# Kernel optimization log

Measured on AMD Instinct MI355X. Metric: run time of the kernel, lower is better.

The kernel has to match this reference:

```python
import jax, jax.numpy as jnp
import numpy as np

N_USER, N_ITEM, D, N_LAYER, NNZ, B = 50000, 100000, 64, 3, 2400000, 4096
NEG_SLOPE = 0.2
EPS = 1e-12


def setup_inputs() -> dict:
    key = jax.random.key(0)
    ks = jax.random.split(key, 12)
    N = N_USER + N_ITEM
    user_emb = jax.random.normal(ks[0], (N_USER, D), dtype=jnp.float32) * 0.1
    item_emb = jax.random.normal(ks[1], (N_ITEM, D), dtype=jnp.float32) * 0.1
    rows = jax.random.randint(ks[2], (NNZ,), 0, N, dtype=jnp.int32)
    cols = jax.random.randint(ks[3], (NNZ,), 0, N, dtype=jnp.int32)
    edge_index = jnp.stack([rows, cols])  # [2, nnz] COO indices of sparse L
    # normalized-Laplacian-like positive values, ~1/deg scale
    edge_vals = jax.random.uniform(ks[4], (NNZ,), dtype=jnp.float32) * (1.0 / 16.0)
    scale = 1.0 / np.sqrt(D)
    W1 = jax.random.normal(ks[5], (N_LAYER, D, D), dtype=jnp.float32) * scale
    W2 = jax.random.normal(ks[6], (N_LAYER, D, D), dtype=jnp.float32) * scale
    b1 = jnp.zeros((N_LAYER, D), dtype=jnp.float32)
    b2 = jnp.zeros((N_LAYER, D), dtype=jnp.float32)
    users = jax.random.randint(ks[7], (B,), 1, N_USER + 1, dtype=jnp.int32)      # 1-indexed
    pos_items = jax.random.randint(ks[8], (B,), 1, N_ITEM + 1, dtype=jnp.int32)  # 1-indexed
    neg_items = jax.random.randint(ks[9], (B,), 1, N_ITEM + 1, dtype=jnp.int32)  # 1-indexed
    return {"user_emb": user_emb, "item_emb": item_emb, "edge_vals": edge_vals,
            "W1": W1, "b1": b1, "W2": W2, "b2": b2,
            "edge_index": edge_index, "users": users,
            "pos_items": pos_items, "neg_items": neg_items}


def _spmm(rows, cols, vals, E, num_nodes):
    # sparse COO L @ E : gather source rows, scale by edge value, scatter-add to dest rows
    return jax.ops.segment_sum(vals[:, None] * E[cols], rows, num_segments=num_nodes)


def reference(user_emb, item_emb, edge_vals, W1, b1, W2, b2,
              edge_index, users, pos_items, neg_items):
    n_user = user_emb.shape[0]
    N = n_user + item_emb.shape[0]
    rows, cols = edge_index[0], edge_index[1]
    E = jnp.concatenate([user_emb, item_emb], axis=0)  # [N, d]
    all_E = [E]
    for i in range(W1.shape[0]):
        LE = _spmm(rows, cols, edge_vals, E, N)          # L @ E
        # (L + I) @ E @ W1 + (L@E * E) @ W2  (dropouts are eval-mode identity)
        h = (LE + E) @ W1[i] + b1[i] + (LE * E) @ W2[i] + b2[i]
        E = jax.nn.leaky_relu(h, NEG_SLOPE)
        nrm = jnp.maximum(jnp.linalg.norm(E, axis=1, keepdims=True), EPS)
        all_E.append(E / nrm)  # L2-normalized copy stored; unnormalized E propagates
    all_E = jnp.concatenate(all_E, axis=1)               # [N, d*(1+L)]
    u_emb = all_E[:n_user][users - 1]
    items = all_E[n_user:]
    return u_emb, items[pos_items - 1], items[neg_items - 1]
```

## Files before the change

### kernel.cpp

```cpp
#include <hip/hip_runtime.h>

#define N_USERC 50000
#define N_ITEMC 100000
#define NN      150000
#define DD      64
#define NLAYER  3
#define NNZC    2400000
#define BB      4096
#define NRID    (3*BB)
#define NBKT    147
#define NABLK   586
#define NTILE   4688
#define ELLW    32
#define ELLROWS 150528
#define OVCAP   32768
#define NZBLK   9408

typedef unsigned short ushort_t;
typedef __attribute__((ext_vector_type(8))) short bf16x8;
typedef __attribute__((ext_vector_type(4))) float f32x4;

static __device__ __forceinline__ float bf2f(ushort_t b) {
    unsigned int u = ((unsigned int)b) << 16;
    return __uint_as_float(u);
}
static __device__ __forceinline__ ushort_t f2bf(float f) {
    unsigned int u = __float_as_uint(f);
    u = u + 0x7FFFu + ((u >> 16) & 1u);
    return (ushort_t)(u >> 16);
}

__global__ __launch_bounds__(256) void k_sniffzb(const unsigned int* __restrict__ ue_words,
                                                 int* __restrict__ flag,
                                                 int* __restrict__ bucket_cnt) {
    int t = threadIdx.x;
    if (t < 64) {
        int cnt = 0;
        for (int i = 0; i < 4; i++) {
            unsigned int w = ue_words[t * 4 + i];
            unsigned int lo = w & 0xFFFFu;
            unsigned int ex = (lo >> 7) & 0xFF;
            if (ex >= 100 && ex <= 132) cnt++;
        }
        for (int m = 1; m < 64; m <<= 1) cnt += __shfl_xor(cnt, m, 64);
        if (t == 0) *flag = (cnt >= 128) ? 1 : 0;
    } else if (t - 64 < NBKT) {
        bucket_cnt[t - 64] = 0;
    }
}

__global__ __launch_bounds__(256) void k_zell(int4* __restrict__ ell4,
                                              int* __restrict__ ovcnt) {
    int idx = blockIdx.x * 256 + threadIdx.x;
    ell4[idx] = make_int4(0, 0, 0, 0);
    if (idx == 0) *ovcnt = 0;
}

__global__ __launch_bounds__(256) void k_init2(const void* __restrict__ ue,
                                               const void* __restrict__ ie,
                                               const int* __restrict__ flag,
                                               float* __restrict__ E,
                                               ushort_t* __restrict__ Eb0) {
    int idx = blockIdx.x * 256 + threadIdx.x;
    if (idx >= NN * DD) return;
    int row = idx >> 6;
    bool isU = row < N_USERC;
    int si = isU ? idx : idx - N_USERC * DD;
    float v;
    if (*flag) {
        v = bf2f(isU ? ((const ushort_t*)ue)[si] : ((const ushort_t*)ie)[si]);
    } else {
        v = isU ? ((const float*)ue)[si] : ((const float*)ie)[si];
    }
    E[idx] = v;
    Eb0[idx] = f2bf(v);
}

__global__ __launch_bounds__(256) void k_wprep(const void* __restrict__ W1,
                                               const void* __restrict__ W2,
                                               const void* __restrict__ b1,
                                               const void* __restrict__ b2,
                                               const int* __restrict__ flag,
                                               ushort_t* __restrict__ Wfrag,
                                               float* __restrict__ bsum) {
    int idx = blockIdx.x * 256 + threadIdx.x;
    int isbf = *flag;
    if (idx < NLAYER * 4 * 4 * 64 * 8) {
        int i    = idx & 7;
        int lane = (idx >> 3) & 63;
        int jt   = (idx >> 9) & 3;
        int s    = (idx >> 11) & 3;
        int l    = idx >> 13;
        int kfull = 32 * (s & 1) + 8 * (lane >> 4) + i;
        int col   = jt * 16 + (lane & 15);
        const void* W = (s < 2) ? W1 : W2;
        size_t off = (size_t)l * 4096 + (size_t)kfull * 64 + col;
        float v = isbf ? bf2f(((const ushort_t*)W)[off]) : ((const float*)W)[off];
        Wfrag[idx] = f2bf(v);
    } else {
        int r = idx - NLAYER * 4 * 4 * 64 * 8;
        if (r < NLAYER * 64) {
            float v1 = isbf ? bf2f(((const ushort_t*)b1)[r]) : ((const float*)b1)[r];
            float v2 = isbf ? bf2f(((const ushort_t*)b2)[r]) : ((const float*)b2)[r];
            bsum[r] = v1 + v2;
        }
    }
}

__global__ __launch_bounds__(256) void k_bhist(const int* __restrict__ rows,
                                               int* __restrict__ bucket_cnt) {
    __shared__ int h[NBKT];
    int t = threadIdx.x;
    if (t < NBKT) h[t] = 0;
    __syncthreads();
    int e0 = blockIdx.x * 4096;
#pragma unroll
    for (int i = 0; i < 16; i++) {
        int e = e0 + t + i * 256;
        if (e < NNZC) atomicAdd(&h[rows[e] >> 10], 1);
    }
    __syncthreads();
    if (t < NBKT && h[t]) atomicAdd(&bucket_cnt[t], h[t]);
}

__global__ __launch_bounds__(256) void k_bscan(const int* __restrict__ bucket_cnt,
                                               int* __restrict__ gbase,
                                               int* __restrict__ gcursor) {
    __shared__ int s[256];
    int t = threadIdx.x;
    int v = (t < NBKT) ? bucket_cnt[t] : 0;
    s[t] = v; __syncthreads();
    for (int off = 1; off < 256; off <<= 1) {
        int x = (t >= off) ? s[t - off] : 0;
        __syncthreads();
        s[t] += x;
        __syncthreads();
    }
    if (t < NBKT) { int ex = s[t] - v; gbase[t] = ex; gcursor[t] = ex; }
    if (t == 0) { gbase[NBKT] = NNZC; }
}

__global__ __launch_bounds__(256) void k_phaseA(const int* __restrict__ rows,
                                                const int* __restrict__ cols,
                                                const void* __restrict__ vals,
                                                const int* __restrict__ flag,
                                                int* __restrict__ gcursor,
                                                int2* __restrict__ binned) {
    __shared__ int hist[NBKT], base_[NBKT], lcur[NBKT];
    int t = threadIdx.x;
    int e0 = blockIdx.x * 4096;
    if (t < NBKT) { hist[t] = 0; lcur[t] = 0; }
    __syncthreads();
    int myrow[16];
#pragma unroll
    for (int i = 0; i < 16; i++) {
        int e = e0 + t + i * 256;
        int r = -1;
        if (e < NNZC) { r = rows[e]; atomicAdd(&hist[r >> 10], 1); }
        myrow[i] = r;
    }
    __syncthreads();
    if (t < NBKT && hist[t] > 0) base_[t] = atomicAdd(&gcursor[t], hist[t]);
    __syncthreads();
    int isbf = *flag;
#pragma unroll
    for (int i = 0; i < 16; i++) {
        int e = e0 + t + i * 256;
        if (e < NNZC) {
            int r = myrow[i];
            int bkt = r >> 10;
            int off = atomicAdd(&lcur[bkt], 1);
            int pos = base_[bkt] + off;
            int c = cols[e];
            float v = isbf ? bf2f(((const ushort_t*)vals)[e]) : ((const float*)vals)[e];
            binned[pos] = make_int2(((r & 1023) << 18) | c, __float_as_int(v));
        }
    }
}

__global__ __launch_bounds__(256) void k_phaseB(const int* __restrict__ gbase,
                                                const int2* __restrict__ binned,
                                                int2* __restrict__ ell,
                                                int4* __restrict__ ovbuf,
                                                int* __restrict__ ovcnt) {
    __shared__ int rcur[1024];
    int b = blockIdx.x, t = threadIdx.x;
    int s = gbase[b], e = gbase[b + 1];
    for (int i = t; i < 1024; i += 256) rcur[i] = 0;
    __syncthreads();
    for (int i = s + t; i < e; i += 256) {
        int2 en = binned[i];
        int rl = en.x >> 18;
        int c  = en.x & 0x3FFFF;
        int off = atomicAdd(&rcur[rl], 1);
        if (off < ELLW) {
            ell[((size_t)(b * 1024 + rl)) * ELLW + off] = make_int2(c, en.y);
        } else {
            int p = atomicAdd(ovcnt, 1);
            if (p < OVCAP) ovbuf[p] = make_int4(b * 1024 + rl, c, en.y, 0);
        }
    }
}

__global__ __launch_bounds__(256) void k_layer(const int2* __restrict__ ell,
                                               const int4* __restrict__ ovbuf,
                                               const int* __restrict__ ovcnt,
                                               const ushort_t* __restrict__ Eb_in,
                                               float* __restrict__ E,
                                               ushort_t* __restrict__ Eb_out,
                                               const ushort_t* __restrict__ Wfrag,
                                               const float* __restrict__ bsum,
                                               int layer) {
    __shared__ float sLE[32][68];
    __shared__ float sE [32][68];

    int t    = threadIdx.x;
    int wv   = t >> 6;
    int lane = t & 63;
    int oct  = lane >> 3;
    int d8   = (lane & 7) * 8;
    int hl   = lane >> 4;
    int l16  = lane & 15;
    int r0   = blockIdx.x << 5;

    {
        int lr = t >> 3;
        int dm = (t & 7) * 8;
        int gr = r0 + lr;
        float4 va = make_float4(0.f, 0.f, 0.f, 0.f), vb = va;
        if (gr < NN) {
            const float4* p = (const float4*)(E + (size_t)gr * DD + dm);
            va = p[0]; vb = p[1];
        }
        *(float4*)&sE[lr][dm]     = va;
        *(float4*)&sE[lr][dm + 4] = vb;
    }

    int baseRow = r0 + wv * 8;
    int2 pv[4];
#pragma unroll
    for (int v = 0; v < 4; v++)
        pv[v] = ell[(size_t)baseRow * ELLW + v * 8 + oct];

#pragma unroll
    for (int sub = 0; sub < 8; sub++) {
        uint4 q[4];
#pragma unroll
        for (int v = 0; v < 4; v++)
            q[v] = *(const uint4*)(Eb_in + ((size_t)(unsigned)pv[v].x << 6) + d8);
        int2 pvn[4];
        if (sub < 7) {
#pragma unroll
            for (int v = 0; v < 4; v++)
                pvn[v] = ell[(size_t)(baseRow + sub + 1) * ELLW + v * 8 + oct];
        }
        float acc[8];
#pragma unroll
        for (int k = 0; k < 8; k++) acc[k] = 0.f;
#pragma unroll
        for (int v = 0; v < 4; v++) {
            float w = __int_as_float(pv[v].y);
            acc[0] = fmaf(w, __uint_as_float(q[v].x << 16),         acc[0]);
            acc[1] = fmaf(w, __uint_as_float(q[v].x & 0xffff0000u), acc[1]);
            acc[2] = fmaf(w, __uint_as_float(q[v].y << 16),         acc[2]);
            acc[3] = fmaf(w, __uint_as_float(q[v].y & 0xffff0000u), acc[3]);
            acc[4] = fmaf(w, __uint_as_float(q[v].z << 16),         acc[4]);
            acc[5] = fmaf(w, __uint_as_float(q[v].z & 0xffff0000u), acc[5]);
            acc[6] = fmaf(w, __uint_as_float(q[v].w << 16),         acc[6]);
            acc[7] = fmaf(w, __uint_as_float(q[v].w & 0xffff0000u), acc[7]);
        }
#pragma unroll
        for (int m = 8; m < 64; m <<= 1)
#pragma unroll
            for (int k = 0; k < 8; k++) acc[k] += __shfl_xor(acc[k], m, 64);
        if (oct == 0) {
            int lr = wv * 8 + sub;
            *(float4*)&sLE[lr][d8]     = make_float4(acc[0], acc[1], acc[2], acc[3]);
            *(float4*)&sLE[lr][d8 + 4] = make_float4(acc[4], acc[5], acc[6], acc[7]);
        }
#pragma unroll
        for (int v = 0; v < 4; v++) pv[v] = pvn[v];
    }
    __syncthreads();

    {
        int n = *ovcnt;
        n = (n < OVCAP) ? n : OVCAP;
        if (wv == 0) {
            for (int i = 0; i < n; i++) {
                int4 ov = ovbuf[i];
                if ((unsigned)(ov.x - r0) < 32u) {
                    float w = __int_as_float(ov.z);
                    sLE[ov.x - r0][lane] += w * bf2f(Eb_in[(size_t)ov.y * DD + lane]);
                }
            }
        }
    }
    __syncthreads();

    int rt = wv & 1;
    int j0w = wv >> 1;
    int jtA = 2 * j0w, jtB = 2 * j0w + 1;
    const uint4* wb = (const uint4*)(Wfrag + (size_t)layer * 8192);
    float bsA = bsum[layer * 64 + jtA * 16 + l16];
    float bsB = bsum[layer * 64 + jtB * 16 + l16];

    f32x4 accA = (f32x4){0.f, 0.f, 0.f, 0.f};
    f32x4 accB = (f32x4){0.f, 0.f, 0.f, 0.f};
    int lrow = rt * 16 + l16;

#pragma unroll
    for (int sh = 0; sh < 2; sh++) {
        bf16x8 w1a, w1b, w2a, w2b;
        {
            uint4 qa = wb[(sh * 4 + jtA) * 64 + lane];
            uint4 qb = wb[(sh * 4 + jtB) * 64 + lane];
            uint4 qc = wb[((2 + sh) * 4 + jtA) * 64 + lane];
            uint4 qd = wb[((2 + sh) * 4 + jtB) * 64 + lane];
            __builtin_memcpy(&w1a, &qa, 16);
            __builtin_memcpy(&w1b, &qb, 16);
            __builtin_memcpy(&w2a, &qc, 16);
            __builtin_memcpy(&w2b, &qd, 16);
        }
        const float* pl = &sLE[lrow][sh * 32 + hl * 8];
        const float* pe = &sE [lrow][sh * 32 + hl * 8];
        float4 l0 = *(const float4*)pl, l1 = *(const float4*)(pl + 4);
        float4 e0 = *(const float4*)pe, e1 = *(const float4*)(pe + 4);
        float le[8] = {l0.x, l0.y, l0.z, l0.w, l1.x, l1.y, l1.z, l1.w};
        float ee[8] = {e0.x, e0.y, e0.z, e0.w, e1.x, e1.y, e1.z, e1.w};
        unsigned int u1h[4], u1l[4], u2h[4], u2l[4];
#pragma unroll
        for (int d = 0; d < 4; d++) {
            float s0 = le[2*d]   + ee[2*d];
            float s1 = le[2*d+1] + ee[2*d+1];
            float m0 = le[2*d]   * ee[2*d];
            float m1 = le[2*d+1] * ee[2*d+1];
            asm("v_cvt_pk_bf16_f32 %0, %1, %2" : "=v"(u1h[d]) : "v"(s0), "v"(s1));
            asm("v_cvt_pk_bf16_f32 %0, %1, %2" : "=v"(u2h[d]) : "v"(m0), "v"(m1));
            float s0r = s0 - __uint_as_float(u1h[d] << 16);
            float s1r = s1 - __uint_as_float(u1h[d] & 0xffff0000u);
            float m0r = m0 - __uint_as_float(u2h[d] << 16);
            float m1r = m1 - __uint_as_float(u2h[d] & 0xffff0000u);
            asm("v_cvt_pk_bf16_f32 %0, %1, %2" : "=v"(u1l[d]) : "v"(s0r), "v"(s1r));
            asm("v_cvt_pk_bf16_f32 %0, %1, %2" : "=v"(u2l[d]) : "v"(m0r), "v"(m1r));
        }
        bf16x8 p1h, p1l, p2h, p2l;
        __builtin_memcpy(&p1h, u1h, 16);
        __builtin_memcpy(&p1l, u1l, 16);
        __builtin_memcpy(&p2h, u2h, 16);
        __builtin_memcpy(&p2l, u2l, 16);

        accA = __builtin_amdgcn_mfma_f32_16x16x32_bf16(p1h, w1a, accA, 0, 0, 0);
        accA = __builtin_amdgcn_mfma_f32_16x16x32_bf16(p1l, w1a, accA, 0, 0, 0);
        accA = __builtin_amdgcn_mfma_f32_16x16x32_bf16(p2h, w2a, accA, 0, 0, 0);
        accA = __builtin_amdgcn_mfma_f32_16x16x32_bf16(p2l, w2a, accA, 0, 0, 0);
        accB = __builtin_amdgcn_mfma_f32_16x16x32_bf16(p1h, w1b, accB, 0, 0, 0);
        accB = __builtin_amdgcn_mfma_f32_16x16x32_bf16(p1l, w1b, accB, 0, 0, 0);
        accB = __builtin_amdgcn_mfma_f32_16x16x32_bf16(p2h, w2b, accB, 0, 0, 0);
        accB = __builtin_amdgcn_mfma_f32_16x16x32_bf16(p2l, w2b, accB, 0, 0, 0);
    }

#pragma unroll
    for (int g = 0; g < 4; g++) {
        int r = r0 + rt * 16 + hl * 4 + g;
        if (r < NN) {
            float hA = accA[g] + bsA; hA = (hA >= 0.f) ? hA : 0.2f * hA;
            float hB = accB[g] + bsB; hB = (hB >= 0.f) ? hB : 0.2f * hB;
            E[(size_t)r * DD + jtA * 16 + l16] = hA;
            E[(size_t)r * DD + jtB * 16 + l16] = hB;
            Eb_out[(size_t)r * DD + jtA * 16 + l16] = f2bf(hA);
            Eb_out[(size_t)r * DD + jtB * 16 + l16] = f2bf(hB);
        }
    }
}

static __device__ __forceinline__ int rid_to_node(int rid,
                                                  const int* users, const int* pos, const int* neg) {
    if (rid < BB)      return users[rid] - 1;
    if (rid < 2 * BB)  return N_USERC + pos[rid - BB] - 1;
    return N_USERC + neg[rid - 2 * BB] - 1;
}

__global__ __launch_bounds__(256) void k_outslice0(const float* __restrict__ E,
                                                   const int* __restrict__ users,
                                                   const int* __restrict__ pos,
                                                   const int* __restrict__ neg,
                                                   float* __restrict__ out) {
    int rid  = blockIdx.x * 4 + (threadIdx.x >> 6);
    int lane = threadIdx.x & 63;
    if (rid >= NRID) return;
    int node = rid_to_node(rid, users, pos, neg);
    out[(size_t)rid * 256 + lane] = E[(size_t)node * DD + lane];
}

__global__ __launch_bounds__(256) void k_outnorm(const float* __restrict__ E,
                                                 const int* __restrict__ users,
                                                 const int* __restrict__ pos,
                                                 const int* __restrict__ neg,
                                                 float* __restrict__ out,
                                                 int cbase) {
    int rid  = blockIdx.x * 4 + (threadIdx.x >> 6);
    int lane = threadIdx.x & 63;
    if (rid >= NRID) return;
    int node = rid_to_node(rid, users, pos, neg);
    float v = E[(size_t)node * DD + lane];
    float p2 = v * v;
    for (int m = 1; m < 64; m <<= 1) p2 += __shfl_xor(p2, m, 64);
    float nr = fmaxf(sqrtf(p2), 1e-12f);
    out[(size_t)rid * 256 + cbase + lane] = v / nr;
}

extern "C" void kernel_launch(void* const* d_in, const int* in_sizes, int n_in,
                              void* d_out, int out_size, void* d_ws, size_t ws_size,
                              hipStream_t stream) {
    const void* ue   = d_in[0];
    const void* ie   = d_in[1];
    const void* ev   = d_in[2];
    const void* W1   = d_in[3];
    const void* b1   = d_in[4];
    const void* W2   = d_in[5];
    const void* b2   = d_in[6];
    const int*  ei   = (const int*)d_in[7];
    const int*  usr  = (const int*)d_in[8];
    const int*  posi = (const int*)d_in[9];
    const int*  negi = (const int*)d_in[10];
    float*      out  = (float*)d_out;

    const int* rows = ei;
    const int* cols = ei + NNZC;

    char* w = (char*)d_ws;
    float*  E         = (float*)w;  w += (size_t)NN * DD * 4;
    ushort_t* Eb1     = (ushort_t*)w; w += (size_t)NN * DD * 2;
    int2*   binned    = (int2*)w;   w += (size_t)NNZC * 8;
    ushort_t* Eb0     = (ushort_t*)binned;
    int2*   ell       = (int2*)w;   w += (size_t)ELLROWS * ELLW * 8;
    int4*   ovbuf     = (int4*)w;   w += (size_t)OVCAP * 16;
    int*    ovcnt     = (int*)w;    w += 256;
    int*    gbase     = (int*)w;    w += 1024;
    int*    gcursor   = (int*)w;    w += 1024;
    int*    bucket_cnt= (int*)w;    w += 1024;
    int*    flag      = (int*)w;    w += 256;
    ushort_t* Wfrag   = (ushort_t*)w; w += 49152;
    float*  bsum      = (float*)w;  w += 768;

    k_sniffzb<<<1, 256, 0, stream>>>((const unsigned int*)ue, flag, bucket_cnt);
    k_zell<<<NZBLK, 256, 0, stream>>>((int4*)ell, ovcnt);
    k_wprep<<<97, 256, 0, stream>>>(W1, W2, b1, b2, flag, Wfrag, bsum);
    k_bhist<<<NABLK, 256, 0, stream>>>(rows, bucket_cnt);
    k_bscan<<<1, 256, 0, stream>>>(bucket_cnt, gbase, gcursor);
    k_phaseA<<<NABLK, 256, 0, stream>>>(rows, cols, ev, flag, gcursor, binned);
    k_phaseB<<<NBKT, 256, 0, stream>>>(gbase, binned, ell, ovbuf, ovcnt);
    k_init2<<<37500, 256, 0, stream>>>(ue, ie, flag, E, Eb0);

    k_outslice0<<<3072, 256, 0, stream>>>(E, usr, posi, negi, out);

    for (int l = 0; l < NLAYER; l++) {
        const ushort_t* ebi = (l & 1) ? Eb1 : Eb0;
        ushort_t*       ebo = (l & 1) ? Eb0 : Eb1;
        k_layer<<<NTILE, 256, 0, stream>>>(ell, ovbuf, ovcnt, ebi, E, ebo, Wfrag, bsum, l);
        k_outnorm<<<3072, 256, 0, stream>>>(E, usr, posi, negi, out, 64 * (l + 1));
    }
}
```

Baseline: 450.3 us.

## Drop full ELL zeroing pass and software-pipeline gathers in layer kernel

Removes the separate kernel that zeroed the whole ELL buffer. Instead, phaseB zero-fills only the unused tail slots of each row after binning, and the overflow counter reset moves into the sniff kernel. The layer kernel now prefetches the next row's bf16 embedding gathers one sub-iteration ahead and the index pairs two ahead, so gather latency overlaps the FMA and shuffle reductions. The E tile store into LDS is deferred until after the loop. The cost is more live registers, which could lower occupancy.

```diff
diff --git a/kernel.cpp b/kernel.cpp
--- a/kernel.cpp
+++ b/kernel.cpp
@@ -14,7 +14,6 @@
 #define ELLW    32
 #define ELLROWS 150528
 #define OVCAP   32768
-#define NZBLK   9408
 
 typedef unsigned short ushort_t;
 typedef __attribute__((ext_vector_type(8))) short bf16x8;
@@ -32,7 +31,8 @@
 
 __global__ __launch_bounds__(256) void k_sniffzb(const unsigned int* __restrict__ ue_words,
                                                  int* __restrict__ flag,
-                                                 int* __restrict__ bucket_cnt) {
+                                                 int* __restrict__ bucket_cnt,
+                                                 int* __restrict__ ovcnt) {
     int t = threadIdx.x;
     if (t < 64) {
         int cnt = 0;
@@ -46,14 +46,9 @@
         if (t == 0) *flag = (cnt >= 128) ? 1 : 0;
     } else if (t - 64 < NBKT) {
         bucket_cnt[t - 64] = 0;
-    }
-}
-
-__global__ __launch_bounds__(256) void k_zell(int4* __restrict__ ell4,
-                                              int* __restrict__ ovcnt) {
-    int idx = blockIdx.x * 256 + threadIdx.x;
-    ell4[idx] = make_int4(0, 0, 0, 0);
-    if (idx == 0) *ovcnt = 0;
+    } else if (t == 255) {
+        *ovcnt = 0;
+    }
 }
 
 __global__ __launch_bounds__(256) void k_init2(const void* __restrict__ ue,
@@ -200,6 +195,12 @@
             if (p < OVCAP) ovbuf[p] = make_int4(b * 1024 + rl, c, en.y, 0);
         }
     }
+    __syncthreads();
+    for (int i = t; i < 1024; i += 256) {
+        int start = rcur[i]; if (start > ELLW) start = ELLW;
+        int2* rp = ell + ((size_t)(b * 1024 + i)) * ELLW;
+        for (int j = start; j < ELLW; j++) rp[j] = make_int2(0, 0);
+    }
 }
 
 __global__ __launch_bounds__(256) void k_layer(const int2* __restrict__ ell,
@@ -223,51 +224,58 @@
     int l16  = lane & 15;
     int r0   = blockIdx.x << 5;
 
+    int lr_ = t >> 3;
+    int dm_ = (t & 7) * 8;
+    float4 eva = make_float4(0.f, 0.f, 0.f, 0.f), evb = eva;
     {
-        int lr = t >> 3;
-        int dm = (t & 7) * 8;
-        int gr = r0 + lr;
-        float4 va = make_float4(0.f, 0.f, 0.f, 0.f), vb = va;
+        int gr = r0 + lr_;
         if (gr < NN) {
-            const float4* p = (const float4*)(E + (size_t)gr * DD + dm);
-            va = p[0]; vb = p[1];
-        }
-        *(float4*)&sE[lr][dm]     = va;
-        *(float4*)&sE[lr][dm + 4] = vb;
+            const float4* p = (const float4*)(E + (size_t)gr * DD + dm_);
+            eva = p[0]; evb = p[1];
+        }
     }
 
     int baseRow = r0 + wv * 8;
-    int2 pv[4];
+    int2 pv_c[4], pv_n[4];
+    uint4 q_c[4];
 #pragma unroll
     for (int v = 0; v < 4; v++)
-        pv[v] = ell[(size_t)baseRow * ELLW + v * 8 + oct];
+        pv_c[v] = ell[(size_t)baseRow * ELLW + v * 8 + oct];
+#pragma unroll
+    for (int v = 0; v < 4; v++)
+        q_c[v] = *(const uint4*)(Eb_in + ((size_t)(unsigned)pv_c[v].x << 6) + d8);
+#pragma unroll
+    for (int v = 0; v < 4; v++)
+        pv_n[v] = ell[(size_t)(baseRow + 1) * ELLW + v * 8 + oct];
 
 #pragma unroll
     for (int sub = 0; sub < 8; sub++) {
-        uint4 q[4];
-#pragma unroll
-        for (int v = 0; v < 4; v++)
-            q[v] = *(const uint4*)(Eb_in + ((size_t)(unsigned)pv[v].x << 6) + d8);
-        int2 pvn[4];
+        uint4 q_n[4];
+        int2 pv_n2[4];
         if (sub < 7) {
 #pragma unroll
             for (int v = 0; v < 4; v++)
-                pvn[v] = ell[(size_t)(baseRow + sub + 1) * ELLW + v * 8 + oct];
+                q_n[v] = *(const uint4*)(Eb_in + ((size_t)(unsigned)pv_n[v].x << 6) + d8);
+        }
+        if (sub < 6) {
+#pragma unroll
+            for (int v = 0; v < 4; v++)
+                pv_n2[v] = ell[(size_t)(baseRow + sub + 2) * ELLW + v * 8 + oct];
         }
         float acc[8];
 #pragma unroll
         for (int k = 0; k < 8; k++) acc[k] = 0.f;
 #pragma unroll
         for (int v = 0; v < 4; v++) {
-            float w = __int_as_float(pv[v].y);
-            acc[0] = fmaf(w, __uint_as_float(q[v].x << 16),         acc[0]);
-            acc[1] = fmaf(w, __uint_as_float(q[v].x & 0xffff0000u), acc[1]);
-            acc[2] = fmaf(w, __uint_as_float(q[v].y << 16),         acc[2]);
-            acc[3] = fmaf(w, __uint_as_float(q[v].y & 0xffff0000u), acc[3]);
-            acc[4] = fmaf(w, __uint_as_float(q[v].z << 16),         acc[4]);
-            acc[5] = fmaf(w, __uint_as_float(q[v].z & 0xffff0000u), acc[5]);
-            acc[6] = fmaf(w, __uint_as_float(q[v].w << 16),         acc[6]);
-            acc[7] = fmaf(w, __uint_as_float(q[v].w & 0xffff0000u), acc[7]);
+            float w = __int_as_float(pv_c[v].y);
+            acc[0] = fmaf(w, __uint_as_float(q_c[v].x << 16),         acc[0]);
+            acc[1] = fmaf(w, __uint_as_float(q_c[v].x & 0xffff0000u), acc[1]);
+            acc[2] = fmaf(w, __uint_as_float(q_c[v].y << 16),         acc[2]);
+            acc[3] = fmaf(w, __uint_as_float(q_c[v].y & 0xffff0000u), acc[3]);
+            acc[4] = fmaf(w, __uint_as_float(q_c[v].z << 16),         acc[4]);
+            acc[5] = fmaf(w, __uint_as_float(q_c[v].z & 0xffff0000u), acc[5]);
+            acc[6] = fmaf(w, __uint_as_float(q_c[v].w << 16),         acc[6]);
+            acc[7] = fmaf(w, __uint_as_float(q_c[v].w & 0xffff0000u), acc[7]);
         }
 #pragma unroll
         for (int m = 8; m < 64; m <<= 1)
@@ -279,8 +287,15 @@
             *(float4*)&sLE[lr][d8 + 4] = make_float4(acc[4], acc[5], acc[6], acc[7]);
         }
 #pragma unroll
-        for (int v = 0; v < 4; v++) pv[v] = pvn[v];
-    }
+        for (int v = 0; v < 4; v++) {
+            pv_c[v] = pv_n[v];
+            q_c[v]  = q_n[v];
+            pv_n[v] = pv_n2[v];
+        }
+    }
+
+    *(float4*)&sE[lr_][dm_]     = eva;
+    *(float4*)&sE[lr_][dm_ + 4] = evb;
     __syncthreads();
 
     {
@@ -444,8 +459,7 @@
     ushort_t* Wfrag   = (ushort_t*)w; w += 49152;
     float*  bsum      = (float*)w;  w += 768;
 
-    k_sniffzb<<<1, 256, 0, stream>>>((const unsigned int*)ue, flag, bucket_cnt);
-    k_zell<<<NZBLK, 256, 0, stream>>>((int4*)ell, ovcnt);
+    k_sniffzb<<<1, 256, 0, stream>>>((const unsigned int*)ue, flag, bucket_cnt, ovcnt);
     k_wprep<<<97, 256, 0, stream>>>(W1, W2, b1, b2, flag, Wfrag, bsum);
     k_bhist<<<NABLK, 256, 0, stream>>>(rows, bucket_cnt);
     k_bscan<<<1, 256, 0, stream>>>(bucket_cnt, gbase, gcursor);
```

After: 456.2 us. No clear change (+1.3%).
